# Kernel tuning notes

Hardware: AMD Instinct MI355X
Metric: run time of the kernel (lower is better)

## Reference

```python
import jax, jax.numpy as jnp
import numpy as np

N = 50000      # nodes per graph (template.shape[1])
DIM = 3        # template.shape[0]
B = 32         # batch of graphs
E = 150000     # edges per graph
BN_EPS = 1e-5


def setup_inputs() -> dict:
    key = jax.random.key(0)
    ks = jax.random.split(key, 24)

    def w(k, shape):
        s = 1.0 / np.sqrt(shape[0])
        return jax.random.normal(k, shape, jnp.float32) * s

    H = 2 * DIM
    inp = {
        "x": jax.random.normal(ks[0], (B * N, DIM), jnp.float32),
        "edge_base": jax.random.randint(ks[1], (2, E), 0, N, dtype=jnp.int32),
        "W1": w(ks[2], (DIM, H)), "b1": jnp.zeros((H,), jnp.float32),
        "g1": jnp.ones((H,), jnp.float32), "be1": jnp.zeros((H,), jnp.float32),
        "W2": w(ks[3], (H, H)), "b2": jnp.zeros((H,), jnp.float32),
        "g2": jnp.ones((H,), jnp.float32), "be2": jnp.zeros((H,), jnp.float32),
        "W3": w(ks[4], (H, H)), "b3": jnp.zeros((H,), jnp.float32),
        "g3": jnp.ones((H,), jnp.float32), "be3": jnp.zeros((H,), jnp.float32),
        "lw1": w(ks[5], (N * H, 256)), "lb1": jnp.zeros((256,), jnp.float32),
        "lw2": w(ks[6], (256, 128)), "lb2": jnp.zeros((128,), jnp.float32),
        "lw3": w(ks[7], (128, 64)), "lb3": jnp.zeros((64,), jnp.float32),
        "lw4": w(ks[8], (64, 32)), "lb4": jnp.zeros((32,), jnp.float32),
        "num_graphs": B,
        "num_nodes": N,
    }
    return inp


def _gcn_norm(edge_base, num_graphs, num_nodes):
    """Batched edge index with self-loops + symmetric GCN normalization."""
    NB = num_graphs * num_nodes
    offsets = (jnp.arange(num_graphs, dtype=jnp.int32) * num_nodes)
    # replicate per-graph edges with node-id offset: [2, B*E]
    ei = (edge_base[:, None, :] + offsets[None, :, None]).reshape(2, -1)
    loop = jnp.arange(NB, dtype=jnp.int32)
    row = jnp.concatenate([ei[0], loop])  # source
    col = jnp.concatenate([ei[1], loop])  # target
    deg = jax.ops.segment_sum(jnp.ones_like(col, jnp.float32), col, num_segments=NB)
    dis = jnp.where(deg > 0, jax.lax.rsqrt(jnp.maximum(deg, 1.0)), 0.0)
    norm = dis[row] * dis[col]
    return row, col, norm, NB


def _gcn_conv(h, row, col, norm, NB, W, b):
    m = h @ W                               # transform then propagate (PyG GCNConv)
    msg = m[row] * norm[:, None]            # gather + scale
    agg = jax.ops.segment_sum(msg, col, num_segments=NB)  # scatter-add
    return agg + b


def _bn(o, g, be):
    mu = o.mean(axis=0)
    var = o.var(axis=0)
    return g * (o - mu) * jax.lax.rsqrt(var + BN_EPS) + be


def reference(x, edge_base, W1, b1, g1, be1, W2, b2, g2, be2, W3, b3, g3, be3,
              lw1, lb1, lw2, lb2, lw3, lb3, lw4, lb4, num_graphs, num_nodes):
    row, col, norm, NB = _gcn_norm(edge_base, num_graphs, num_nodes)
    o = jax.nn.relu(_bn(_gcn_conv(x, row, col, norm, NB, W1, b1), g1, be1))
    o = jax.nn.relu(_bn(_gcn_conv(o, row, col, norm, NB, W2, b2), g2, be2))
    o = jax.nn.relu(_bn(_gcn_conv(o, row, col, norm, NB, W3, b3), g3, be3))
    o = o.reshape(num_graphs, -1)           # [B, N*2*dim]
    o = jax.nn.relu(o @ lw1 + lb1)
    o = jax.nn.relu(o @ lw2 + lb2)
    o = jax.nn.relu(o @ lw3 + lb3)
    return o @ lw4 + lb4                    # [B, 32]
```

## Files before the change

kernel.cpp:

```cpp
#include <hip/hip_runtime.h>

#define NNODES 50000
#define BGR 32
#define ROWF 192
#define BN_EPS 1e-5f
#define NC 50
#define GSPLITS (NNODES / NC)
#define RGROUPS 16
#define GATHER_BLOCKS 1024

__device__ inline unsigned int bf16rne(float x) {
    unsigned int u = __float_as_uint(x);
    return (u + 0x7FFFu + ((u >> 16) & 1u)) >> 16;
}
__device__ inline unsigned int bf16pack(float a, float b) {
    return bf16rne(a) | (bf16rne(b) << 16);
}
__device__ inline float4 ldrow_bf16(const unsigned short* p) {
    uint2 q = *(const uint2*)p;
    float4 v;
    v.x = __uint_as_float(q.x << 16);
    v.y = __uint_as_float(q.x & 0xFFFF0000u);
    v.z = __uint_as_float(q.y << 16);
    v.w = __uint_as_float(q.y & 0xFFFF0000u);
    return v;
}

__global__ void count_deg_kernel(const int* __restrict__ col, int E, int* __restrict__ deg) {
    int e = blockIdx.x * blockDim.x + threadIdx.x;
    if (e < E) atomicAdd(&deg[col[e]], 1);
}

__global__ void make_dis_kernel(const int* __restrict__ deg, float* __restrict__ dis, int N) {
    int n = blockIdx.x * blockDim.x + threadIdx.x;
    if (n < N) dis[n] = rsqrtf((float)(deg[n] + 1));
}

__global__ __launch_bounds__(256) void scanA_kernel(const int* __restrict__ deg, int* __restrict__ bsum, int N) {
    __shared__ int lds[256];
    int i = blockIdx.x * 256 + threadIdx.x;
    lds[threadIdx.x] = (i < N) ? deg[i] : 0;
    __syncthreads();
    for (int off = 128; off > 0; off >>= 1) {
        if (threadIdx.x < off) lds[threadIdx.x] += lds[threadIdx.x + off];
        __syncthreads();
    }
    if (threadIdx.x == 0) bsum[blockIdx.x] = lds[0];
}

__global__ __launch_bounds__(256) void scanB_kernel(const int* __restrict__ bsum, int* __restrict__ bbase,
                                                    int* __restrict__ offsN, int nblk) {
    __shared__ int lds[256];
    int t = threadIdx.x;
    int v = (t < nblk) ? bsum[t] : 0;
    lds[t] = v;
    __syncthreads();
    for (int off = 1; off < 256; off <<= 1) {
        int u = (t >= off) ? lds[t - off] : 0;
        __syncthreads();
        lds[t] += u;
        __syncthreads();
    }
    if (t < nblk) bbase[t] = lds[t] - v;
    if (t == 255) offsN[0] = lds[255];
}

__global__ __launch_bounds__(256) void scanC_kernel(const int* __restrict__ deg, const int* __restrict__ bbase,
                                                    int* __restrict__ offs, int* __restrict__ cursor, int N) {
    __shared__ int lds[256];
    int i = blockIdx.x * 256 + threadIdx.x;
    int t = threadIdx.x;
    int v = (i < N) ? deg[i] : 0;
    lds[t] = v;
    __syncthreads();
    for (int off = 1; off < 256; off <<= 1) {
        int u = (t >= off) ? lds[t - off] : 0;
        __syncthreads();
        lds[t] += u;
        __syncthreads();
    }
    if (i < N) {
        int excl = bbase[blockIdx.x] + lds[t] - v;
        offs[i] = excl;
        cursor[i] = excl;
    }
}

__global__ void fill_csr_kernel(const int* __restrict__ row, const int* __restrict__ col,
                                const float* __restrict__ dis, int* __restrict__ cursor,
                                int2* __restrict__ csr_rw, int E) {
    int e = blockIdx.x * blockDim.x + threadIdx.x;
    if (e >= E) return;
    int r = row[e], c = col[e];
    int pos = atomicAdd(&cursor[c], 1);
    csr_rw[pos] = make_int2(r, __float_as_int(dis[r] * dis[c]));
}

__global__ __launch_bounds__(256) void t1_kernel(const float* __restrict__ x,
                                                 const float* __restrict__ W,
                                                 unsigned short* __restrict__ m, int N) {
    __shared__ float xt[BGR][ROWF];
    __shared__ float sW[18];
    int tid = threadIdx.x;
    if (tid < 18) sW[tid] = W[tid];
    int n0 = blockIdx.x * 64;
    int nval = N - n0; if (nval > 64) nval = 64;
    int lim = nval * 3;
    for (int b = 0; b < BGR; b++) {
        if (tid < lim) xt[b][tid] = x[((size_t)b * N + n0) * 3 + tid];
    }
    __syncthreads();
    for (int i = 0; i < 8; i++) {
        int pi = i * 256 + tid;
        int nl = pi >> 5, b = pi & 31;
        if (nl < nval) {
            float h0 = xt[b][nl * 3], h1 = xt[b][nl * 3 + 1], h2 = xt[b][nl * 3 + 2];
            float o[6];
            #pragma unroll
            for (int j = 0; j < 6; j++)
                o[j] = h0 * sW[j] + h1 * sW[6 + j] + h2 * sW[12 + j];
            unsigned int* mp = (unsigned int*)(m + (size_t)(n0 + nl) * ROWF + b * 6);
            mp[0] = bf16pack(o[0], o[1]);
            mp[1] = bf16pack(o[2], o[3]);
            mp[2] = bf16pack(o[4], o[5]);
        }
    }
}

__global__ __launch_bounds__(256) void t23_kernel(const unsigned short* __restrict__ agg,
                                                  const float* __restrict__ stats,
                                                  const float* __restrict__ gam,
                                                  const float* __restrict__ bet,
                                                  const float* __restrict__ W,
                                                  unsigned short* __restrict__ m, int NB) {
    __shared__ float sW[36];
    int tid = threadIdx.x;
    if (tid < 36) sW[tid] = W[tid];
    __syncthreads();
    float inv = 1.f / (float)NB;
    float sa[6], sc[6];
    #pragma unroll
    for (int j = 0; j < 6; j++) {
        float mu = stats[j] * inv;
        float var = stats[6 + j] * inv - mu * mu;
        float rs = rsqrtf(var + BN_EPS);
        float a = gam[j] * rs;
        sa[j] = a; sc[j] = bet[j] - mu * a;
    }
    size_t i = (size_t)blockIdx.x * 256 + tid;
    if (i >= (size_t)NB) return;
    const unsigned int* ap = (const unsigned int*)(agg + i * 6);
    unsigned int q0 = ap[0], q1 = ap[1], q2 = ap[2];
    float h[6];
    h[0] = __uint_as_float(q0 << 16); h[1] = __uint_as_float(q0 & 0xFFFF0000u);
    h[2] = __uint_as_float(q1 << 16); h[3] = __uint_as_float(q1 & 0xFFFF0000u);
    h[4] = __uint_as_float(q2 << 16); h[5] = __uint_as_float(q2 & 0xFFFF0000u);
    #pragma unroll
    for (int k = 0; k < 6; k++) {
        float v = fmaf(sa[k], h[k], sc[k]);
        h[k] = v > 0.f ? v : 0.f;
    }
    float o[6];
    #pragma unroll
    for (int j = 0; j < 6; j++) {
        float t = 0.f;
        #pragma unroll
        for (int k = 0; k < 6; k++) t = fmaf(h[k], sW[k * 6 + j], t);
        o[j] = t;
    }
    unsigned int* mp = (unsigned int*)(m + i * 6);
    mp[0] = bf16pack(o[0], o[1]);
    mp[1] = bf16pack(o[2], o[3]);
    mp[2] = bf16pack(o[4], o[5]);
}

__global__ __launch_bounds__(256) void gather_kernel(const unsigned short* __restrict__ m,
                                                     const int* __restrict__ offs,
                                                     const int2* __restrict__ csr_rw,
                                                     const float* __restrict__ dis,
                                                     unsigned short* __restrict__ agg,
                                                     float* __restrict__ stats_out, int N) {
    int tid = threadIdx.x;
    int wv = tid >> 6, lane = tid & 63;
    bool lact = lane < 48;
    int loff = lane * 4;
    float4 ssum = make_float4(0.f, 0.f, 0.f, 0.f);
    float4 ssq  = make_float4(0.f, 0.f, 0.f, 0.f);
    int ngrp = (N + 7) >> 3;
    for (int grp = blockIdx.x; grp < ngrp; grp += gridDim.x) {
        int n0 = grp * 8 + wv;
        int n1 = n0 + 4;
        if (n0 >= N) continue;
        bool v1 = (n1 < N);
        float d0 = dis[n0];
        float d1 = v1 ? dis[n1] : 0.f;
        int s0 = offs[n0], e0 = offs[n0 + 1];
        int s1 = v1 ? offs[n1] : 0, e1 = v1 ? offs[n1 + 1] : 0;
        float4 acc0 = make_float4(0.f, 0.f, 0.f, 0.f);
        float4 acc1 = make_float4(0.f, 0.f, 0.f, 0.f);
        if (lact) {
            const float4 va = ldrow_bf16(m + (size_t)n0 * ROWF + loff);
            const float4 vb = ldrow_bf16(m + (size_t)(v1 ? n1 : n0) * ROWF + loff);
            float wa = d0 * d0, wb = d1 * d1;
            acc0.x = wa * va.x; acc0.y = wa * va.y; acc0.z = wa * va.z; acc0.w = wa * va.w;
            acc1.x = wb * vb.x; acc1.y = wb * vb.y; acc1.z = wb * vb.z; acc1.w = wb * vb.w;
        }
        int p0 = s0, p1 = s1;
        int len0 = e0 - s0, len1 = e1 - s1;
        int iters = len0 > len1 ? len0 : len1;
        for (int it = 0; it < iters; it++) {
            int  r0 = n0; float w0 = 0.f;
            int  r1 = v1 ? n1 : n0; float w1 = 0.f;
            if (p0 < e0) { int2 t0 = csr_rw[p0]; r0 = t0.x; w0 = __int_as_float(t0.y); }
            if (p1 < e1) { int2 t1 = csr_rw[p1]; r1 = t1.x; w1 = __int_as_float(t1.y); }
            if (lact) {
                const float4 va = ldrow_bf16(m + (size_t)r0 * ROWF + loff);
                const float4 vb = ldrow_bf16(m + (size_t)r1 * ROWF + loff);
                acc0.x = fmaf(w0, va.x, acc0.x); acc0.y = fmaf(w0, va.y, acc0.y);
                acc0.z = fmaf(w0, va.z, acc0.z); acc0.w = fmaf(w0, va.w, acc0.w);
                acc1.x = fmaf(w1, vb.x, acc1.x); acc1.y = fmaf(w1, vb.y, acc1.y);
                acc1.z = fmaf(w1, vb.z, acc1.z); acc1.w = fmaf(w1, vb.w, acc1.w);
            }
            p0++; p1++;
        }
        if (lact) {
            *(uint2*)(agg + (size_t)n0 * ROWF + loff) =
                make_uint2(bf16pack(acc0.x, acc0.y), bf16pack(acc0.z, acc0.w));
            if (v1)
                *(uint2*)(agg + (size_t)n1 * ROWF + loff) =
                    make_uint2(bf16pack(acc1.x, acc1.y), bf16pack(acc1.z, acc1.w));
        }
        ssum.x += acc0.x + acc1.x; ssum.y += acc0.y + acc1.y;
        ssum.z += acc0.z + acc1.z; ssum.w += acc0.w + acc1.w;
        ssq.x = fmaf(acc0.x, acc0.x, fmaf(acc1.x, acc1.x, ssq.x));
        ssq.y = fmaf(acc0.y, acc0.y, fmaf(acc1.y, acc1.y, ssq.y));
        ssq.z = fmaf(acc0.z, acc0.z, fmaf(acc1.z, acc1.z, ssq.z));
        ssq.w = fmaf(acc0.w, acc0.w, fmaf(acc1.w, acc1.w, ssq.w));
    }
    float vals[8] = {ssum.x, ssum.y, ssum.z, ssum.w, ssq.x, ssq.y, ssq.z, ssq.w};
    #pragma unroll
    for (int q = 0; q < 8; q++) {
        vals[q] += __shfl_down(vals[q], 24, 64);
        vals[q] += __shfl_down(vals[q], 12, 64);
        vals[q] += __shfl_down(vals[q], 6, 64);
        vals[q] += __shfl_down(vals[q], 3, 64);
    }
    __shared__ float red[4][3][8];
    if (lane < 3) {
        #pragma unroll
        for (int q = 0; q < 8; q++) red[wv][lane][q] = vals[q];
    }
    __syncthreads();
    if (tid < 24) {
        int l0 = tid >> 3, qq = tid & 7;
        float v = red[0][l0][qq] + red[1][l0][qq] + red[2][l0][qq] + red[3][l0][qq];
        int j = (4 * l0 + (qq & 3)) % 6;
        atomicAdd(&stats_out[(qq < 4 ? 0 : 6) + j], v);
    }
}

__global__ __launch_bounds__(256) void gemm1_kernel(const unsigned short* __restrict__ agg3,
                                                    const float* __restrict__ stats,
                                                    const float* __restrict__ gam,
                                                    const float* __restrict__ bet,
                                                    const float* __restrict__ lw1,
                                                    float* __restrict__ partials, int NB) {
    __shared__ float s_act[NC * ROWF];
    int tid = threadIdx.x;
    float inv = 1.f / (float)NB;
    float sa[6], sc[6];
    #pragma unroll
    for (int j = 0; j < 6; j++) {
        float mu = stats[j] * inv;
        float var = stats[6 + j] * inv - mu * mu;
        float rs = rsqrtf(var + BN_EPS);
        float a = gam[j] * rs;
        sa[j] = a; sc[j] = bet[j] - mu * a;
    }
    int n0 = blockIdx.x * NC;
    const unsigned int* ab = (const unsigned int*)(agg3 + (size_t)n0 * ROWF);
    for (int idx = tid; idx < NC * ROWF / 2; idx += 256) {
        unsigned int q = ab[idx];
        float v0 = __uint_as_float(q << 16);
        float v1 = __uint_as_float(q & 0xFFFF0000u);
        int j0 = (2 * idx) % 6;
        float t0 = fmaf(sa[j0], v0, sc[j0]);
        float t1 = fmaf(sa[j0 + 1], v1, sc[j0 + 1]);
        s_act[2 * idx]     = t0 > 0.f ? t0 : 0.f;
        s_act[2 * idx + 1] = t1 > 0.f ? t1 : 0.f;
    }
    __syncthreads();
    int wv = tid >> 6, lane = tid & 63;
    int b0 = wv * 8;
    float4 acc[8];
    #pragma unroll
    for (int i = 0; i < 8; i++) acc[i] = make_float4(0.f, 0.f, 0.f, 0.f);
    const float* wbase = lw1 + (size_t)n0 * 6 * 256 + 4 * lane;
    for (int nl = 0; nl < NC; nl++) {
        float4 w6[6];
        #pragma unroll
        for (int j = 0; j < 6; j++)
            w6[j] = *(const float4*)(wbase + ((size_t)nl * 6 + j) * 256);
        const float* hb = &s_act[nl * ROWF + b0 * 6];
        #pragma unroll
        for (int bb = 0; bb < 8; bb++) {
            const float* hp = hb + bb * 6;
            float2 h01 = *(const float2*)hp;
            float2 h23 = *(const float2*)(hp + 2);
            float2 h45 = *(const float2*)(hp + 4);
            float4 a = acc[bb];
            a.x = fmaf(h01.x, w6[0].x, a.x); a.y = fmaf(h01.x, w6[0].y, a.y);
            a.z = fmaf(h01.x, w6[0].z, a.z); a.w = fmaf(h01.x, w6[0].w, a.w);
            a.x = fmaf(h01.y, w6[1].x, a.x); a.y = fmaf(h01.y, w6[1].y, a.y);
            a.z = fmaf(h01.y, w6[1].z, a.z); a.w = fmaf(h01.y, w6[1].w, a.w);
            a.x = fmaf(h23.x, w6[2].x, a.x); a.y = fmaf(h23.x, w6[2].y, a.y);
            a.z = fmaf(h23.x, w6[2].z, a.z); a.w = fmaf(h23.x, w6[2].w, a.w);
            a.x = fmaf(h23.y, w6[3].x, a.x); a.y = fmaf(h23.y, w6[3].y, a.y);
            a.z = fmaf(h23.y, w6[3].z, a.z); a.w = fmaf(h23.y, w6[3].w, a.w);
            a.x = fmaf(h45.x, w6[4].x, a.x); a.y = fmaf(h45.x, w6[4].y, a.y);
            a.z = fmaf(h45.x, w6[4].z, a.z); a.w = fmaf(h45.x, w6[4].w, a.w);
            a.x = fmaf(h45.y, w6[5].x, a.x); a.y = fmaf(h45.y, w6[5].y, a.y);
            a.z = fmaf(h45.y, w6[5].z, a.z); a.w = fmaf(h45.y, w6[5].w, a.w);
            acc[bb] = a;
        }
    }
    #pragma unroll
    for (int bb = 0; bb < 8; bb++)
        *(float4*)&partials[(((size_t)blockIdx.x * BGR) + b0 + bb) * 256 + 4 * lane] = acc[bb];
}

__global__ __launch_bounds__(256) void reduce1_kernel(const float* __restrict__ partials,
                                                      float* __restrict__ p2) {
    int o = blockIdx.x * 256 + threadIdx.x;
    int g = blockIdx.y;
    float a = 0.f;
    for (int s = g; s < GSPLITS; s += RGROUPS)
        a += partials[(size_t)s * (BGR * 256) + o];
    p2[g * (BGR * 256) + o] = a;
}

__global__ __launch_bounds__(1024) void tail_kernel(const float* __restrict__ p2,
                                                    const float* __restrict__ lb1,
                                                    const float* __restrict__ lw2, const float* __restrict__ lb2,
                                                    const float* __restrict__ lw3, const float* __restrict__ lb3,
                                                    const float* __restrict__ lw4, const float* __restrict__ lb4,
                                                    float* __restrict__ out) {
    __shared__ float red[4][256];
    __shared__ float s1[256], s2[128], s3[64];
    int b = blockIdx.x;
    int tid = threadIdx.x;
    int c = tid & 255, sg = tid >> 8;
    float a = 0.f;
    for (int g = sg; g < RGROUPS; g += 4)
        a += p2[g * (BGR * 256) + b * 256 + c];
    red[sg][c] = a;
    __syncthreads();
    if (tid < 256) {
        float v = red[0][tid] + red[1][tid] + red[2][tid] + red[3][tid] + lb1[tid];
        s1[tid] = v > 0.f ? v : 0.f;
    }
    __syncthreads();
    if (tid < 128) {
        float acc = lb2[tid];
        for (int k = 0; k < 256; k++) acc += s1[k] * lw2[k * 128 + tid];
        s2[tid] = acc > 0.f ? acc : 0.f;
    }
    __syncthreads();
    if (tid < 64) {
        float acc = lb3[tid];
        for (int k = 0; k < 128; k++) acc += s2[k] * lw3[k * 64 + tid];
        s3[tid] = acc > 0.f ? acc : 0.f;
    }
    __syncthreads();
    if (tid < 32) {
        float acc = lb4[tid];
        for (int k = 0; k < 64; k++) acc += s3[k] * lw4[k * 32 + tid];
        out[b * 32 + tid] = acc;
    }
}

extern "C" void kernel_launch(void* const* d_in, const int* in_sizes, int n_in,
                              void* d_out, int out_size, void* d_ws, size_t ws_size,
                              hipStream_t stream) {
    const float* x   = (const float*)d_in[0];
    const int* edge  = (const int*)d_in[1];
    const float* W1  = (const float*)d_in[2];
    const float* g1  = (const float*)d_in[4];
    const float* be1 = (const float*)d_in[5];
    const float* W2  = (const float*)d_in[6];
    const float* g2  = (const float*)d_in[8];
    const float* be2 = (const float*)d_in[9];
    const float* W3  = (const float*)d_in[10];
    const float* g3  = (const float*)d_in[12];
    const float* be3 = (const float*)d_in[13];
    const float* lw1 = (const float*)d_in[14];
    const float* lb1 = (const float*)d_in[15];
    const float* lw2 = (const float*)d_in[16];
    const float* lb2 = (const float*)d_in[17];
    const float* lw3 = (const float*)d_in[18];
    const float* lb3 = (const float*)d_in[19];
    const float* lw4 = (const float*)d_in[20];
    const float* lb4 = (const float*)d_in[21];

    const int E = in_sizes[1] / 2;
    const int N = NNODES;
    const int B = in_sizes[0] / (N * 3);
    const int NB = B * N;
    const int nblk = (N + 255) / 256;

    char* ws = (char*)d_ws;
    size_t rowShorts = (size_t)N * ROWF * sizeof(unsigned short);
    unsigned short* aggbuf = (unsigned short*)ws;
    unsigned short* mbuf   = (unsigned short*)(ws + rowShorts);
    float* partials = (float*)(ws + 2 * rowShorts);
    char* p = ws + 2 * rowShorts + (size_t)GSPLITS * BGR * 256 * 4;
    float* dis    = (float*)p;  p += (size_t)N * 4;
    int*   deg    = (int*)p;    p += (size_t)N * 4;
    int*   offs   = (int*)p;    p += (size_t)(N + 1) * 4;
    int*   cursor = (int*)p;    p += (size_t)N * 4;
    int*   bsum   = (int*)p;    p += 256 * 4;
    int*   bbase  = (int*)p;    p += 256 * 4;
    int2*  csr_rw = (int2*)p;   p += (size_t)E * 8;
    float* stats  = (float*)p;  p += 48 * 4;
    float* p2     = (float*)p;  p += (size_t)RGROUPS * BGR * 256 * 4;
    float* stats1 = stats, *stats2 = stats + 16, *stats3 = stats + 32;

    const int T = 256;

    hipMemsetAsync(deg, 0, (size_t)N * 4, stream);
    hipMemsetAsync(stats, 0, 48 * 4, stream);
    count_deg_kernel<<<(E + T - 1) / T, T, 0, stream>>>(edge + E, E, deg);
    make_dis_kernel<<<(N + T - 1) / T, T, 0, stream>>>(deg, dis, N);
    scanA_kernel<<<nblk, T, 0, stream>>>(deg, bsum, N);
    scanB_kernel<<<1, T, 0, stream>>>(bsum, bbase, offs + N, nblk);
    scanC_kernel<<<nblk, T, 0, stream>>>(deg, bbase, offs, cursor, N);
    fill_csr_kernel<<<(E + T - 1) / T, T, 0, stream>>>(edge, edge + E, dis, cursor, csr_rw, E);

    t1_kernel<<<(N + 63) / 64, T, 0, stream>>>(x, W1, mbuf, N);
    gather_kernel<<<GATHER_BLOCKS, T, 0, stream>>>(mbuf, offs, csr_rw, dis, aggbuf, stats1, N);
    t23_kernel<<<(NB + T - 1) / T, T, 0, stream>>>(aggbuf, stats1, g1, be1, W2, mbuf, NB);
    gather_kernel<<<GATHER_BLOCKS, T, 0, stream>>>(mbuf, offs, csr_rw, dis, aggbuf, stats2, N);
    t23_kernel<<<(NB + T - 1) / T, T, 0, stream>>>(aggbuf, stats2, g2, be2, W3, mbuf, NB);
    gather_kernel<<<GATHER_BLOCKS, T, 0, stream>>>(mbuf, offs, csr_rw, dis, aggbuf, stats3, N);

    gemm1_kernel<<<GSPLITS, T, 0, stream>>>(aggbuf, stats3, g3, be3, lw1, partials, NB);
    reduce1_kernel<<<dim3(32, RGROUPS), T, 0, stream>>>(partials, p2);
    tail_kernel<<<B, 1024, 0, stream>>>(p2, lb1, lw2, lb2, lw3, lb3, lw4, lb4, (float*)d_out);
}
```

Measured before the change: 438.5 us.

## Store gemm1 activations and split-K partials in bf16, double node chunk size

Each gemm1 block now covers 100 nodes instead of 50, halving the number of blocks and partial outputs. Normalized activations in shared memory are packed as bf16 pairs so the larger chunk fits in LDS, and split-K partials are written as packed bf16, with reduce1 unpacking them and running half as many blocks. This cuts partial-sum write and read traffic and per-block overhead. In exchange it loses precision in the activations and in the partial sums, and gives fewer blocks for parallelism.

```diff
diff --git a/kernel.cpp b/kernel.cpp
--- a/kernel.cpp
+++ b/kernel.cpp
@@ -4,7 +4,7 @@
 #define BGR 32
 #define ROWF 192
 #define BN_EPS 1e-5f
-#define NC 50
+#define NC 100
 #define GSPLITS (NNODES / NC)
 #define RGROUPS 16
 #define GATHER_BLOCKS 1024
@@ -264,8 +264,8 @@
                                                     const float* __restrict__ gam,
                                                     const float* __restrict__ bet,
                                                     const float* __restrict__ lw1,
-                                                    float* __restrict__ partials, int NB) {
-    __shared__ float s_act[NC * ROWF];
+                                                    unsigned int* __restrict__ partials, int NB) {
+    __shared__ unsigned int s_act[NC * ROWF / 2];
     int tid = threadIdx.x;
     float inv = 1.f / (float)NB;
     float sa[6], sc[6];
@@ -286,8 +286,9 @@
         int j0 = (2 * idx) % 6;
         float t0 = fmaf(sa[j0], v0, sc[j0]);
         float t1 = fmaf(sa[j0 + 1], v1, sc[j0 + 1]);
-        s_act[2 * idx]     = t0 > 0.f ? t0 : 0.f;
-        s_act[2 * idx + 1] = t1 > 0.f ? t1 : 0.f;
+        t0 = t0 > 0.f ? t0 : 0.f;
+        t1 = t1 > 0.f ? t1 : 0.f;
+        s_act[idx] = bf16pack(t0, t1);
     }
     __syncthreads();
     int wv = tid >> 6, lane = tid & 63;
@@ -301,42 +302,49 @@
         #pragma unroll
         for (int j = 0; j < 6; j++)
             w6[j] = *(const float4*)(wbase + ((size_t)nl * 6 + j) * 256);
-        const float* hb = &s_act[nl * ROWF + b0 * 6];
+        const unsigned int* hu = &s_act[nl * (ROWF / 2) + b0 * 3];
         #pragma unroll
         for (int bb = 0; bb < 8; bb++) {
-            const float* hp = hb + bb * 6;
-            float2 h01 = *(const float2*)hp;
-            float2 h23 = *(const float2*)(hp + 2);
-            float2 h45 = *(const float2*)(hp + 4);
+            unsigned int q0 = hu[bb * 3], q1 = hu[bb * 3 + 1], q2 = hu[bb * 3 + 2];
+            float h0 = __uint_as_float(q0 << 16), h1 = __uint_as_float(q0 & 0xFFFF0000u);
+            float h2 = __uint_as_float(q1 << 16), h3 = __uint_as_float(q1 & 0xFFFF0000u);
+            float h4 = __uint_as_float(q2 << 16), h5 = __uint_as_float(q2 & 0xFFFF0000u);
             float4 a = acc[bb];
-            a.x = fmaf(h01.x, w6[0].x, a.x); a.y = fmaf(h01.x, w6[0].y, a.y);
-            a.z = fmaf(h01.x, w6[0].z, a.z); a.w = fmaf(h01.x, w6[0].w, a.w);
-            a.x = fmaf(h01.y, w6[1].x, a.x); a.y = fmaf(h01.y, w6[1].y, a.y);
-            a.z = fmaf(h01.y, w6[1].z, a.z); a.w = fmaf(h01.y, w6[1].w, a.w);
-            a.x = fmaf(h23.x, w6[2].x, a.x); a.y = fmaf(h23.x, w6[2].y, a.y);
-            a.z = fmaf(h23.x, w6[2].z, a.z); a.w = fmaf(h23.x, w6[2].w, a.w);
-            a.x = fmaf(h23.y, w6[3].x, a.x); a.y = fmaf(h23.y, w6[3].y, a.y);
-            a.z = fmaf(h23.y, w6[3].z, a.z); a.w = fmaf(h23.y, w6[3].w, a.w);
-            a.x = fmaf(h45.x, w6[4].x, a.x); a.y = fmaf(h45.x, w6[4].y, a.y);
-            a.z = fmaf(h45.x, w6[4].z, a.z); a.w = fmaf(h45.x, w6[4].w, a.w);
-            a.x = fmaf(h45.y, w6[5].x, a.x); a.y = fmaf(h45.y, w6[5].y, a.y);
-            a.z = fmaf(h45.y, w6[5].z, a.z); a.w = fmaf(h45.y, w6[5].w, a.w);
+            a.x = fmaf(h0, w6[0].x, a.x); a.y = fmaf(h0, w6[0].y, a.y);
+            a.z = fmaf(h0, w6[0].z, a.z); a.w = fmaf(h0, w6[0].w, a.w);
+            a.x = fmaf(h1, w6[1].x, a.x); a.y = fmaf(h1, w6[1].y, a.y);
+            a.z = fmaf(h1, w6[1].z, a.z); a.w = fmaf(h1, w6[1].w, a.w);
+            a.x = fmaf(h2, w6[2].x, a.x); a.y = fmaf(h2, w6[2].y, a.y);
+            a.z = fmaf(h2, w6[2].z, a.z); a.w = fmaf(h2, w6[2].w, a.w);
+            a.x = fmaf(h3, w6[3].x, a.x); a.y = fmaf(h3, w6[3].y, a.y);
+            a.z = fmaf(h3, w6[3].z, a.z); a.w = fmaf(h3, w6[3].w, a.w);
+            a.x = fmaf(h4, w6[4].x, a.x); a.y = fmaf(h4, w6[4].y, a.y);
+            a.z = fmaf(h4, w6[4].z, a.z); a.w = fmaf(h4, w6[4].w, a.w);
+            a.x = fmaf(h5, w6[5].x, a.x); a.y = fmaf(h5, w6[5].y, a.y);
+            a.z = fmaf(h5, w6[5].z, a.z); a.w = fmaf(h5, w6[5].w, a.w);
             acc[bb] = a;
         }
     }
     #pragma unroll
-    for (int bb = 0; bb < 8; bb++)
-        *(float4*)&partials[(((size_t)blockIdx.x * BGR) + b0 + bb) * 256 + 4 * lane] = acc[bb];
-}
-
-__global__ __launch_bounds__(256) void reduce1_kernel(const float* __restrict__ partials,
+    for (int bb = 0; bb < 8; bb++) {
+        unsigned int* prow = partials + (((size_t)blockIdx.x * BGR) + b0 + bb) * 128;
+        *(uint2*)&prow[2 * lane] = make_uint2(bf16pack(acc[bb].x, acc[bb].y),
+                                             bf16pack(acc[bb].z, acc[bb].w));
+    }
+}
+
+__global__ __launch_bounds__(256) void reduce1_kernel(const unsigned int* __restrict__ partials,
                                                       float* __restrict__ p2) {
     int o = blockIdx.x * 256 + threadIdx.x;
     int g = blockIdx.y;
-    float a = 0.f;
-    for (int s = g; s < GSPLITS; s += RGROUPS)
-        a += partials[(size_t)s * (BGR * 256) + o];
-    p2[g * (BGR * 256) + o] = a;
+    float a0 = 0.f, a1 = 0.f;
+    for (int s = g; s < GSPLITS; s += RGROUPS) {
+        unsigned int q = partials[(size_t)s * (BGR * 128) + o];
+        a0 += __uint_as_float(q << 16);
+        a1 += __uint_as_float(q & 0xFFFF0000u);
+    }
+    p2[(size_t)g * (BGR * 256) + 2 * o]     = a0;
+    p2[(size_t)g * (BGR * 256) + 2 * o + 1] = a1;
 }
 
 __global__ __launch_bounds__(1024) void tail_kernel(const float* __restrict__ p2,
@@ -352,7 +360,7 @@
     int c = tid & 255, sg = tid >> 8;
     float a = 0.f;
     for (int g = sg; g < RGROUPS; g += 4)
-        a += p2[g * (BGR * 256) + b * 256 + c];
+        a += p2[(size_t)g * (BGR * 256) + b * 256 + c];
     red[sg][c] = a;
     __syncthreads();
     if (tid < 256) {
@@ -412,8 +420,8 @@
     size_t rowShorts = (size_t)N * ROWF * sizeof(unsigned short);
     unsigned short* aggbuf = (unsigned short*)ws;
     unsigned short* mbuf   = (unsigned short*)(ws + rowShorts);
-    float* partials = (float*)(ws + 2 * rowShorts);
-    char* p = ws + 2 * rowShorts + (size_t)GSPLITS * BGR * 256 * 4;
+    unsigned int* partials = (unsigned int*)(ws + 2 * rowShorts);
+    char* p = ws + 2 * rowShorts + (size_t)GSPLITS * BGR * 128 * 4;
     float* dis    = (float*)p;  p += (size_t)N * 4;
     int*   deg    = (int*)p;    p += (size_t)N * 4;
     int*   offs   = (int*)p;    p += (size_t)(N + 1) * 4;
@@ -444,6 +452,6 @@
     gather_kernel<<<GATHER_BLOCKS, T, 0, stream>>>(mbuf, offs, csr_rw, dis, aggbuf, stats3, N);
 
     gemm1_kernel<<<GSPLITS, T, 0, stream>>>(aggbuf, stats3, g3, be3, lw1, partials, NB);
-    reduce1_kernel<<<dim3(32, RGROUPS), T, 0, stream>>>(partials, p2);
+    reduce1_kernel<<<dim3(16, RGROUPS), T, 0, stream>>>(partials, p2);
     tail_kernel<<<B, 1024, 0, stream>>>(p2, lb1, lw2, lb2, lw3, lb3, lw4, lb4, (float*)d_out);
 }
```

Result: slower. 488.6 us (+11.4%).
